# Performance work log

Measured on AMD Instinct MI355X. Metric: run time of the kernel, lower is better.

The kernel has to match this reference:

```python
import jax, jax.numpy as jnp
import numpy as np

B, T, D = 64, 128, 1024
E = 2048      # embedding_dim of state encoder
CD = 256      # VQ code_dim
NC = 1024     # num_codes
BETA = 0.25   # commitment cost


def setup_inputs() -> dict:
    key = jax.random.key(0)
    ks = jax.random.split(key, 5)
    states = jax.random.normal(ks[0], (B, T, D), dtype=jnp.float32)
    next_states = jax.random.normal(ks[1], (B, T, D), dtype=jnp.float32)
    # VarianceScaling(scale=2.0, fan_in) init
    W_s = jax.random.normal(ks[2], (D, E), dtype=jnp.float32) * np.sqrt(2.0 / D)
    b_s = jnp.zeros((E,), dtype=jnp.float32)
    W_p = jax.random.normal(ks[3], (2 * E, CD), dtype=jnp.float32) * np.sqrt(2.0 / (2 * E))
    b_p = jnp.zeros((CD,), dtype=jnp.float32)
    codebook = jax.random.normal(ks[4], (NC, CD), dtype=jnp.float32)
    return {"states": states, "next_states": next_states, "W_s": W_s,
            "b_s": b_s, "W_p": W_p, "b_p": b_p, "codebook": codebook}


def reference(states, next_states, W_s, b_s, W_p, b_p, codebook):
    # dual state encoder (shared weights)
    se = states @ W_s + b_s            # (B,T,E)
    ne = next_states @ W_s + b_s       # (B,T,E)
    policy_input = jax.nn.gelu(jnp.concatenate([se, ne], axis=-1))  # (B,T,2E)
    latent = policy_input @ W_p + b_p  # (B,T,CD)

    # --- VectorQuantizerEMA forward ---
    flat = latent.reshape(-1, CD)      # (N, CD), N = B*T
    # squared euclidean distances to codebook rows
    dists = (jnp.sum(flat * flat, axis=1, keepdims=True)
             - 2.0 * flat @ codebook.T
             + jnp.sum(codebook * codebook, axis=1))  # (N, NC)
    idx = jnp.argmin(dists, axis=1)                    # (N,)
    encodings = jax.nn.one_hot(idx, NC, dtype=latent.dtype)  # (N, NC)
    quantize = codebook[idx].reshape(latent.shape)     # (B,T,CD)

    e_latent_loss = jnp.mean(jnp.square(jax.lax.stop_gradient(quantize) - latent))
    loss = BETA * e_latent_loss
    # straight-through estimator
    quantize_st = latent + jax.lax.stop_gradient(quantize - latent)

    avg_probs = jnp.mean(encodings, axis=0)
    perplexity = jnp.exp(-jnp.sum(avg_probs * jnp.log(avg_probs + 1e-10)))

    encodings = encodings.reshape(B, T, NC)
    encoding_indices = idx.reshape(B, T)
    return quantize_st, loss, perplexity, encodings, encoding_indices
```

## Files before the change

kernel.cpp:

```cpp
#include <hip/hip_runtime.h>

#define NROW  8192
#define D_    1024
#define E_    2048
#define P2E_  4096
#define CD_   256
#define NC_   1024
#define BETA_ 0.25f
#define SPLITK 8

typedef __attribute__((ext_vector_type(8))) short short8;
typedef __attribute__((ext_vector_type(4))) float f32x4;

__device__ __forceinline__ ushort f2bf(float x) {
    union { float f; unsigned u; } v; v.f = x;
    unsigned r = (v.u + 0x7fffu + ((v.u >> 16) & 1u)) >> 16;
    return (ushort)r;
}
__device__ __forceinline__ float bf2f(ushort h) {
    union { unsigned u; float f; } v; v.u = ((unsigned)h) << 16;
    return v.f;
}
__device__ __forceinline__ void split2(float x, ushort& h, ushort& l) {
    h = f2bf(x);
    l = f2bf(x - bf2f(h));
}
__device__ __forceinline__ float gelu_tanh(float x) {
    float x3 = x * x * x;
    return 0.5f * x * (1.0f + tanhf(0.7978845608028654f * (x + 0.044715f * x3)));
}

#define GLD16(gp, lp) __builtin_amdgcn_global_load_lds( \
    (const __attribute__((address_space(1))) void*)(gp), \
    (__attribute__((address_space(3))) void*)(lp), 16, 0, 0)

template<int EPI>
__global__ __launch_bounds__(256)
void gemm_bf16x3(const ushort* __restrict__ Ah, const ushort* __restrict__ Al,
                 const ushort* __restrict__ Bh, const ushort* __restrict__ Bl,
                 int K, int ksteps,
                 const float* __restrict__ bias,
                 float* __restrict__ outF,
                 ushort* __restrict__ oPh, ushort* __restrict__ oPl,
                 const float* __restrict__ cn,
                 float* __restrict__ candv, int* __restrict__ candi)
{
    __shared__ alignas(16) ushort sAh[4096], sAl[4096], sBh[4096], sBl[4096];
    const int t = threadIdx.x;
    const int l = t & 63;
    const int w = t >> 6;
    const int wr = w >> 1, wc = w & 1;

    const int nxy = gridDim.x * gridDim.y;
    const int id  = blockIdx.y * gridDim.x + blockIdx.x;
    const int swz = (id & 7) * (nxy >> 3) + (id >> 3);
    const int bx  = swz % gridDim.x;
    const int by  = swz / gridDim.x;

    const int bm = by * 128;
    const int bn = bx * 128;
    const int kstart = (EPI == 1) ? (int)blockIdx.z * (ksteps * 32) : 0;

    const int srow = t >> 2;
    const int scol = ((t & 3) ^ ((t >> 3) & 3)) * 8;
    const ushort* gAh = Ah + (size_t)(bm + srow) * K + kstart + scol;
    const ushort* gAl = Al + (size_t)(bm + srow) * K + kstart + scol;
    const ushort* gBh = Bh + (size_t)(bn + srow) * K + kstart + scol;
    const ushort* gBl = Bl + (size_t)(bn + srow) * K + kstart + scol;
    const size_t rstep = (size_t)64 * K;
    const int lo0 = t * 8, lo1 = t * 8 + 2048;

    f32x4 acc[4][4];
#pragma unroll
    for (int i = 0; i < 4; i++)
#pragma unroll
        for (int j = 0; j < 4; j++) acc[i][j] = (f32x4)0.0f;

    const int rsw = ((l >> 4) ^ (((l & 15) >> 1) & 3)) * 8;
    const int ar = (wr * 64 + (l & 15)) * 32 + rsw;
    const int br = (wc * 64 + (l & 15)) * 32 + rsw;

#define STAGE8() do { \
        GLD16(gAh, &sAh[lo0]); GLD16(gAh + rstep, &sAh[lo1]); \
        GLD16(gAl, &sAl[lo0]); GLD16(gAl + rstep, &sAl[lo1]); \
        GLD16(gBh, &sBh[lo0]); GLD16(gBh + rstep, &sBh[lo1]); \
        GLD16(gBl, &sBl[lo0]); GLD16(gBl + rstep, &sBl[lo1]); \
    } while (0)

    STAGE8();
    __syncthreads();

    for (int s = 0; s < ksteps; ++s) {
        short8 fah[4], fal[4], fbh[4], fbl[4];
#pragma unroll
        for (int i = 0; i < 4; i++) {
            fah[i] = *(const short8*)&sAh[ar + i * 16 * 32];
            fal[i] = *(const short8*)&sAl[ar + i * 16 * 32];
            fbh[i] = *(const short8*)&sBh[br + i * 16 * 32];
            fbl[i] = *(const short8*)&sBl[br + i * 16 * 32];
        }
        __syncthreads();

        if (s + 1 < ksteps) {
            gAh += 32; gAl += 32; gBh += 32; gBl += 32;
            STAGE8();
        }

        __builtin_amdgcn_s_setprio(1);
#pragma unroll
        for (int i = 0; i < 4; i++)
#pragma unroll
            for (int j = 0; j < 4; j++) {
                acc[i][j] = __builtin_amdgcn_mfma_f32_16x16x32_bf16(fah[i], fbh[j], acc[i][j], 0, 0, 0);
                acc[i][j] = __builtin_amdgcn_mfma_f32_16x16x32_bf16(fah[i], fbl[j], acc[i][j], 0, 0, 0);
                acc[i][j] = __builtin_amdgcn_mfma_f32_16x16x32_bf16(fal[i], fbh[j], acc[i][j], 0, 0, 0);
            }
        __builtin_amdgcn_s_setprio(0);
        __syncthreads();
    }
#undef STAGE8

    if constexpr (EPI == 2) {
        float (*redv)[2] = (float(*)[2])sAh;
        int   (*redi)[2] = (int(*)[2])sAl;
        float cnv[4];
#pragma unroll
        for (int j = 0; j < 4; j++) cnv[j] = cn[bn + wc * 64 + j * 16 + (l & 15)];
#pragma unroll
        for (int i = 0; i < 4; i++) {
            const int grow = bm + wr * 64 + i * 16 + (l >> 4) * 4;
#pragma unroll
            for (int r = 0; r < 4; r++) {
                float bv = INFINITY; int bi = 0;
#pragma unroll
                for (int j = 0; j < 4; j++) {
                    float d = cnv[j] - 2.0f * acc[i][j][r];
                    int c = bn + wc * 64 + j * 16 + (l & 15);
                    if (d < bv) { bv = d; bi = c; }
                }
#pragma unroll
                for (int m = 1; m < 16; m <<= 1) {
                    float ov = __shfl_xor(bv, m, 64);
                    int   oi = __shfl_xor(bi, m, 64);
                    if (ov < bv || (ov == bv && oi < bi)) { bv = ov; bi = oi; }
                }
                int rl = wr * 64 + i * 16 + (l >> 4) * 4 + r;
                if ((l & 15) == 0) { redv[rl][wc] = bv; redi[rl][wc] = bi; }
#pragma unroll
                for (int j = 0; j < 4; j++)
                    outF[(size_t)(grow + r) * NC_ + bn + wc * 64 + j * 16 + (l & 15)] = 0.0f;
            }
        }
        __syncthreads();
        if (t < 128) {
            float v0 = redv[t][0], v1 = redv[t][1];
            int   i0 = redi[t][0], i1 = redi[t][1];
            bool take1 = (v1 < v0) || (v1 == v0 && i1 < i0);
            candv[(size_t)(bm + t) * 8 + bx] = take1 ? v1 : v0;
            candi[(size_t)(bm + t) * 8 + bx] = take1 ? i1 : i0;
        }
        return;
    }

#pragma unroll
    for (int i = 0; i < 4; i++) {
        const int grow = bm + wr * 64 + i * 16 + (l >> 4) * 4;
#pragma unroll
        for (int j = 0; j < 4; j++) {
            const int gcol = bn + wc * 64 + j * 16 + (l & 15);
            f32x4 a = acc[i][j];
            if constexpr (EPI == 0) {
                const float bb = bias[gcol];
#pragma unroll
                for (int r = 0; r < 4; r++) {
                    int m = grow + r;
                    float x = gelu_tanh(a[r] + bb);
                    ushort h, lo; split2(x, h, lo);
                    int pr = (m < NROW) ? m : m - NROW;
                    int pc = ((m < NROW) ? 0 : E_) + gcol;
                    oPh[(size_t)pr * P2E_ + pc] = h;
                    oPl[(size_t)pr * P2E_ + pc] = lo;
                }
            } else if constexpr (EPI == 1) {
                float* o = outF + ((size_t)NROW * blockIdx.z + grow) * CD_ + gcol;
#pragma unroll
                for (int r = 0; r < 4; r++) o[(size_t)r * CD_] = a[r];
            }
        }
    }
}

__global__ void split_k(const float* __restrict__ in, ushort* __restrict__ oh,
                        ushort* __restrict__ ol, int n4)
{
    int i = blockIdx.x * blockDim.x + threadIdx.x;
    int stride = gridDim.x * blockDim.x;
    for (; i < n4; i += stride) {
        float4 v = ((const float4*)in)[i];
        ushort4 h, lo;
        split2(v.x, h.x, lo.x); split2(v.y, h.y, lo.y);
        split2(v.z, h.z, lo.z); split2(v.w, h.w, lo.w);
        ((ushort4*)oh)[i] = h;
        ((ushort4*)ol)[i] = lo;
    }
}

__global__ __launch_bounds__(1024)
void tsplit_k(const float* __restrict__ in, ushort* __restrict__ oh,
              ushort* __restrict__ ol, int R, int C)
{
    __shared__ float tile[32][33];
    int c0 = blockIdx.x * 32, r0 = blockIdx.y * 32;
    int tx = threadIdx.x, ty = threadIdx.y;
    tile[ty][tx] = in[(size_t)(r0 + ty) * C + c0 + tx];
    __syncthreads();
    float x = tile[tx][ty];
    ushort h, lo; split2(x, h, lo);
    size_t o = (size_t)(c0 + ty) * R + r0 + tx;
    oh[o] = h; ol[o] = lo;
}

__global__ __launch_bounds__(256)
void combine_k(const float* __restrict__ part, const float* __restrict__ bias,
               float* __restrict__ latent, ushort* __restrict__ lh,
               ushort* __restrict__ ll)
{
    int row = blockIdx.x, t = threadIdx.x;
    float x = bias[t];
#pragma unroll
    for (int z = 0; z < SPLITK; z++) x += part[((size_t)z * NROW + row) * CD_ + t];
    latent[(size_t)row * CD_ + t] = x;
    ushort h, lo; split2(x, h, lo);
    lh[(size_t)row * CD_ + t] = h;
    ll[(size_t)row * CD_ + t] = lo;
}

__global__ __launch_bounds__(256) void row_norms(const float* __restrict__ X,
                                                 float* __restrict__ out)
{
    __shared__ float s[256];
    int n = blockIdx.x, t = threadIdx.x;
    float v = X[(size_t)n * 256 + t];
    s[t] = v * v;
    __syncthreads();
    for (int st = 128; st > 0; st >>= 1) {
        if (t < st) s[t] += s[t + st];
        __syncthreads();
    }
    if (t == 0) out[n] = s[0];
}

__global__ void zero_hist(int* hist) { hist[threadIdx.x] = 0; }

__global__ __launch_bounds__(256) void vq2_kernel(
    const float* __restrict__ latent, const float* __restrict__ cb,
    const float* __restrict__ candv, const int* __restrict__ candi,
    float* __restrict__ out_enc, float* __restrict__ out_q,
    float* __restrict__ out_idx, int* __restrict__ hist, float* __restrict__ lpart)
{
    __shared__ float sd[256];
    __shared__ int sbc;
    const int n = blockIdx.x, t = threadIdx.x;
    if (t == 0) {
        const float* cv = candv + (size_t)n * 8;
        const int*   ci = candi + (size_t)n * 8;
        float bv = cv[0]; int bi = ci[0];
#pragma unroll
        for (int k = 1; k < 8; k++) {
            float v = cv[k]; int x = ci[k];
            if (v < bv || (v == bv && x < bi)) { bv = v; bi = x; }
        }
        sbc = bi;
    }
    __syncthreads();
    const int bc = sbc;
    if (t == 0) out_enc[(size_t)n * NC_ + bc] = 1.0f;

    float lv = latent[(size_t)n * CD_ + t];
    float q  = cb[(size_t)bc * CD_ + t];
    out_q[(size_t)n * CD_ + t] = lv + (q - lv);
    float diff = q - lv;
    sd[t] = diff * diff;
    __syncthreads();
    for (int st = 128; st > 0; st >>= 1) {
        if (t < st) sd[t] += sd[t + st];
        __syncthreads();
    }
    if (t == 0) {
        lpart[n] = sd[0];
        atomicAdd(&hist[bc], 1);
        out_idx[n] = (float)bc;
    }
}

__global__ __launch_bounds__(1024) void finalize_kernel(
    const float* __restrict__ lpart, const int* __restrict__ hist,
    float* __restrict__ out_loss, float* __restrict__ out_perp)
{
    __shared__ float s[1024];
    int t = threadIdx.x;
    float x = 0.0f;
    for (int i = t; i < NROW; i += 1024) x += lpart[i];
    s[t] = x;
    __syncthreads();
    for (int st = 512; st > 0; st >>= 1) {
        if (t < st) s[t] += s[t + st];
        __syncthreads();
    }
    float total = s[0];
    __syncthreads();
    float p = (float)hist[t] * (1.0f / NROW);
    s[t] = p * logf(p + 1e-10f);
    __syncthreads();
    for (int st = 512; st > 0; st >>= 1) {
        if (t < st) s[t] += s[t + st];
        __syncthreads();
    }
    if (t == 0) {
        *out_loss = BETA_ * (total / (float)((size_t)NROW * CD_));
        *out_perp = expf(-s[0]);
    }
}

extern "C" void kernel_launch(void* const* d_in, const int* in_sizes, int n_in,
                              void* d_out, int out_size, void* d_ws, size_t ws_size,
                              hipStream_t stream)
{
    const float* states      = (const float*)d_in[0];
    const float* next_states = (const float*)d_in[1];
    const float* W_s         = (const float*)d_in[2];
    const float* b_s         = (const float*)d_in[3];
    const float* W_p         = (const float*)d_in[4];
    const float* b_p         = (const float*)d_in[5];
    const float* codebook    = (const float*)d_in[6];

    float* out      = (float*)d_out;
    float* out_q    = out;
    float* out_loss = out + (size_t)NROW * CD_;
    float* out_perp = out_loss + 1;
    float* out_enc  = out_perp + 1;
    float* out_idx  = out_enc + (size_t)NROW * NC_;

    char* ws = (char*)d_ws;
    size_t off = 0;
    auto alloc = [&](size_t bytes) { void* p = ws + off; off += (bytes + 255) & ~255ull; return p; };

    ushort* A1h  = (ushort*)alloc((size_t)2 * NROW * D_ * 2);
    ushort* A1l  = (ushort*)alloc((size_t)2 * NROW * D_ * 2);
    ushort* WsTh = (ushort*)alloc((size_t)E_ * D_ * 2);
    ushort* WsTl = (ushort*)alloc((size_t)E_ * D_ * 2);
    ushort* WpTh = (ushort*)alloc((size_t)CD_ * P2E_ * 2);
    ushort* WpTl = (ushort*)alloc((size_t)CD_ * P2E_ * 2);
    ushort* cbh  = (ushort*)alloc((size_t)NC_ * CD_ * 2);
    ushort* cbl  = (ushort*)alloc((size_t)NC_ * CD_ * 2);
    ushort* Ph   = (ushort*)alloc((size_t)NROW * P2E_ * 2);
    ushort* Pl   = (ushort*)alloc((size_t)NROW * P2E_ * 2);
    ushort* lath = (ushort*)alloc((size_t)NROW * CD_ * 2);
    ushort* latl = (ushort*)alloc((size_t)NROW * CD_ * 2);
    float*  cbn  = (float*)alloc(NC_ * 4);
    int*    hist = (int*)alloc(NC_ * 4);
    float*  lpart= (float*)alloc(NROW * 4);
    float*  candv= (float*)alloc((size_t)NROW * 8 * 4);
    int*    candi= (int*)alloc((size_t)NROW * 8 * 4);
    float* lat_part = (float*)A1h;
    float* latent   = (float*)WsTh;

    {
        int n4 = NROW * D_ / 4;
        split_k<<<2048, 256, 0, stream>>>(states, A1h, A1l, n4);
        split_k<<<2048, 256, 0, stream>>>(next_states, A1h + (size_t)NROW * D_,
                                          A1l + (size_t)NROW * D_, n4);
    }
    tsplit_k<<<dim3(E_ / 32, D_ / 32), dim3(32, 32), 0, stream>>>(W_s, WsTh, WsTl, D_, E_);
    tsplit_k<<<dim3(CD_ / 32, P2E_ / 32), dim3(32, 32), 0, stream>>>(W_p, WpTh, WpTl, P2E_, CD_);
    split_k<<<256, 256, 0, stream>>>(codebook, cbh, cbl, NC_ * CD_ / 4);
    row_norms<<<NC_, 256, 0, stream>>>(codebook, cbn);

    gemm_bf16x3<0><<<dim3(E_ / 128, 2 * NROW / 128), 256, 0, stream>>>(
        A1h, A1l, WsTh, WsTl, D_, D_ / 32, b_s, nullptr, Ph, Pl, nullptr, nullptr, nullptr);

    gemm_bf16x3<1><<<dim3(CD_ / 128, NROW / 128, SPLITK), 256, 0, stream>>>(
        Ph, Pl, WpTh, WpTl, P2E_, P2E_ / 32 / SPLITK, nullptr, lat_part, nullptr, nullptr,
        nullptr, nullptr, nullptr);

    combine_k<<<NROW, 256, 0, stream>>>(lat_part, b_p, latent, lath, latl);

    gemm_bf16x3<2><<<dim3(NC_ / 128, NROW / 128), 256, 0, stream>>>(
        lath, latl, cbh, cbl, CD_, CD_ / 32, nullptr, out_enc, nullptr, nullptr,
        cbn, candv, candi);

    zero_hist<<<1, NC_, 0, stream>>>(hist);
    vq2_kernel<<<NROW, 256, 0, stream>>>(latent, codebook, candv, candi,
                                         out_enc, out_q, out_idx, hist, lpart);
    finalize_kernel<<<1, 1024, 0, stream>>>(lpart, hist, out_loss, out_perp);
}
```

Measured before the change: 359.2 us.

## Widen GEMM tiles to 128x256 with 512 threads and triple-buffered LDS pipeline

Rewrites the split-bf16 GEMM to use 8 waves over a 128x256 output tile and a three-stage LDS ring buffer. Global-to-LDS loads are issued two k-steps ahead and gated with explicit vmcnt waits and raw barriers, replacing the previous single-buffer load/sync pattern. The wider tile also halves the number of argmin candidates per row, so the candidate buffers and the VQ reduction shrink to 4 entries. This is meant to hide memory latency and improve B-tile reuse, at the cost of 144KB of LDS per block and hand-tuned waitcnt values that have to match the number of loads issued.

After: 389.9 us. 1.09x slower.

```diff
diff --git a/kernel.cpp b/kernel.cpp
--- a/kernel.cpp
+++ b/kernel.cpp
@@ -35,21 +35,22 @@
     (__attribute__((address_space(3))) void*)(lp), 16, 0, 0)
 
 template<int EPI>
-__global__ __launch_bounds__(256)
-void gemm_bf16x3(const ushort* __restrict__ Ah, const ushort* __restrict__ Al,
-                 const ushort* __restrict__ Bh, const ushort* __restrict__ Bl,
-                 int K, int ksteps,
-                 const float* __restrict__ bias,
-                 float* __restrict__ outF,
-                 ushort* __restrict__ oPh, ushort* __restrict__ oPl,
-                 const float* __restrict__ cn,
-                 float* __restrict__ candv, int* __restrict__ candi)
-{
-    __shared__ alignas(16) ushort sAh[4096], sAl[4096], sBh[4096], sBl[4096];
+__global__ __launch_bounds__(512, 2)
+void gemm3t(const ushort* __restrict__ Ah, const ushort* __restrict__ Al,
+            const ushort* __restrict__ Bh, const ushort* __restrict__ Bl,
+            int K, int ksteps,
+            const float* __restrict__ bias,
+            float* __restrict__ outF,
+            ushort* __restrict__ oPh, ushort* __restrict__ oPl,
+            const float* __restrict__ cn,
+            float* __restrict__ candv, int* __restrict__ candi)
+{
+    __shared__ alignas(16) ushort lds[3][24576];
     const int t = threadIdx.x;
     const int l = t & 63;
     const int w = t >> 6;
-    const int wr = w >> 1, wc = w & 1;
+    const int wm = w >> 2;
+    const int wn = w & 3;
 
     const int nxy = gridDim.x * gridDim.y;
     const int id  = blockIdx.y * gridDim.x + blockIdx.x;
@@ -58,7 +59,7 @@
     const int by  = swz / gridDim.x;
 
     const int bm = by * 128;
-    const int bn = bx * 128;
+    const int bn = bx * 256;
     const int kstart = (EPI == 1) ? (int)blockIdx.z * (ksteps * 32) : 0;
 
     const int srow = t >> 2;
@@ -67,8 +68,8 @@
     const ushort* gAl = Al + (size_t)(bm + srow) * K + kstart + scol;
     const ushort* gBh = Bh + (size_t)(bn + srow) * K + kstart + scol;
     const ushort* gBl = Bl + (size_t)(bn + srow) * K + kstart + scol;
-    const size_t rstep = (size_t)64 * K;
-    const int lo0 = t * 8, lo1 = t * 8 + 2048;
+    const size_t rstep = (size_t)128 * K;
+    const int d8 = t * 8;
 
     f32x4 acc[4][4];
 #pragma unroll
@@ -76,35 +77,47 @@
 #pragma unroll
         for (int j = 0; j < 4; j++) acc[i][j] = (f32x4)0.0f;
 
-    const int rsw = ((l >> 4) ^ (((l & 15) >> 1) & 3)) * 8;
-    const int ar = (wr * 64 + (l & 15)) * 32 + rsw;
-    const int br = (wc * 64 + (l & 15)) * 32 + rsw;
-
-#define STAGE8() do { \
-        GLD16(gAh, &sAh[lo0]); GLD16(gAh + rstep, &sAh[lo1]); \
-        GLD16(gAl, &sAl[lo0]); GLD16(gAl + rstep, &sAl[lo1]); \
-        GLD16(gBh, &sBh[lo0]); GLD16(gBh + rstep, &sBh[lo1]); \
-        GLD16(gBl, &sBl[lo0]); GLD16(gBl + rstep, &sBl[lo1]); \
+    const int kq = l >> 4, lr = l & 15;
+    const int rsw = (kq ^ ((lr >> 1) & 3)) * 8;
+    int aoff[4], boff[4];
+#pragma unroll
+    for (int i = 0; i < 4; i++) aoff[i] = (wm * 64 + i * 16 + lr) * 32 + rsw;
+#pragma unroll
+    for (int j = 0; j < 4; j++) boff[j] = 8192 + (wn * 64 + j * 16 + lr) * 32 + rsw;
+
+#define STG(b) do { \
+        GLD16(gAh, &lds[b][d8]); \
+        GLD16(gAl, &lds[b][4096 + d8]); \
+        GLD16(gBh, &lds[b][8192 + d8]);  GLD16(gBh + rstep, &lds[b][12288 + d8]); \
+        GLD16(gBl, &lds[b][16384 + d8]); GLD16(gBl + rstep, &lds[b][20480 + d8]); \
+        gAh += 32; gAl += 32; gBh += 32; gBl += 32; \
     } while (0)
 
-    STAGE8();
-    __syncthreads();
-
+    STG(0);
+    STG(1);
     for (int s = 0; s < ksteps; ++s) {
+        const int cb = s % 3;
+        if (s + 2 < ksteps) STG((s + 2) % 3);
+        const int rem = ksteps - 1 - s;
+        if (rem >= 2)      asm volatile("s_waitcnt vmcnt(12)" ::: "memory");
+        else if (rem == 1) asm volatile("s_waitcnt vmcnt(6)"  ::: "memory");
+        else               asm volatile("s_waitcnt vmcnt(0)"  ::: "memory");
+        __builtin_amdgcn_s_barrier();
+        __builtin_amdgcn_sched_barrier(0);
+
         short8 fah[4], fal[4], fbh[4], fbl[4];
 #pragma unroll
         for (int i = 0; i < 4; i++) {
-            fah[i] = *(const short8*)&sAh[ar + i * 16 * 32];
-            fal[i] = *(const short8*)&sAl[ar + i * 16 * 32];
-            fbh[i] = *(const short8*)&sBh[br + i * 16 * 32];
-            fbl[i] = *(const short8*)&sBl[br + i * 16 * 32];
-        }
-        __syncthreads();
-
-        if (s + 1 < ksteps) {
-            gAh += 32; gAl += 32; gBh += 32; gBl += 32;
-            STAGE8();
-        }
+            fah[i] = *(const short8*)&lds[cb][aoff[i]];
+            fal[i] = *(const short8*)&lds[cb][4096 + aoff[i]];
+        }
+#pragma unroll
+        for (int j = 0; j < 4; j++) {
+            fbh[j] = *(const short8*)&lds[cb][boff[j]];
+            fbl[j] = *(const short8*)&lds[cb][8192 + boff[j]];
+        }
+        asm volatile("s_waitcnt lgkmcnt(0)" ::: "memory");
+        __builtin_amdgcn_sched_barrier(0);
 
         __builtin_amdgcn_s_setprio(1);
 #pragma unroll
@@ -116,26 +129,27 @@
                 acc[i][j] = __builtin_amdgcn_mfma_f32_16x16x32_bf16(fal[i], fbh[j], acc[i][j], 0, 0, 0);
             }
         __builtin_amdgcn_s_setprio(0);
-        __syncthreads();
-    }
-#undef STAGE8
+        __builtin_amdgcn_s_barrier();
+        __builtin_amdgcn_sched_barrier(0);
+    }
+#undef STG
 
     if constexpr (EPI == 2) {
-        float (*redv)[2] = (float(*)[2])sAh;
-        int   (*redi)[2] = (int(*)[2])sAl;
+        float (*redv)[4] = (float(*)[4])&lds[0][0];
+        int   (*redi)[4] = (int(*)[4])&lds[0][1024];
         float cnv[4];
 #pragma unroll
-        for (int j = 0; j < 4; j++) cnv[j] = cn[bn + wc * 64 + j * 16 + (l & 15)];
+        for (int j = 0; j < 4; j++) cnv[j] = cn[bn + wn * 64 + j * 16 + lr];
 #pragma unroll
         for (int i = 0; i < 4; i++) {
-            const int grow = bm + wr * 64 + i * 16 + (l >> 4) * 4;
+            const int grow = bm + wm * 64 + i * 16 + kq * 4;
 #pragma unroll
             for (int r = 0; r < 4; r++) {
                 float bv = INFINITY; int bi = 0;
 #pragma unroll
                 for (int j = 0; j < 4; j++) {
                     float d = cnv[j] - 2.0f * acc[i][j][r];
-                    int c = bn + wc * 64 + j * 16 + (l & 15);
+                    int c = bn + wn * 64 + j * 16 + lr;
                     if (d < bv) { bv = d; bi = c; }
                 }
 #pragma unroll
@@ -144,30 +158,33 @@
                     int   oi = __shfl_xor(bi, m, 64);
                     if (ov < bv || (ov == bv && oi < bi)) { bv = ov; bi = oi; }
                 }
-                int rl = wr * 64 + i * 16 + (l >> 4) * 4 + r;
-                if ((l & 15) == 0) { redv[rl][wc] = bv; redi[rl][wc] = bi; }
+                int rl = wm * 64 + i * 16 + kq * 4 + r;
+                if (lr == 0) { redv[rl][wn] = bv; redi[rl][wn] = bi; }
 #pragma unroll
                 for (int j = 0; j < 4; j++)
-                    outF[(size_t)(grow + r) * NC_ + bn + wc * 64 + j * 16 + (l & 15)] = 0.0f;
+                    outF[(size_t)(grow + r) * NC_ + bn + wn * 64 + j * 16 + lr] = 0.0f;
             }
         }
         __syncthreads();
         if (t < 128) {
-            float v0 = redv[t][0], v1 = redv[t][1];
-            int   i0 = redi[t][0], i1 = redi[t][1];
-            bool take1 = (v1 < v0) || (v1 == v0 && i1 < i0);
-            candv[(size_t)(bm + t) * 8 + bx] = take1 ? v1 : v0;
-            candi[(size_t)(bm + t) * 8 + bx] = take1 ? i1 : i0;
+            float bv = redv[t][0]; int bi = redi[t][0];
+#pragma unroll
+            for (int k = 1; k < 4; k++) {
+                float v = redv[t][k]; int x = redi[t][k];
+                if (v < bv || (v == bv && x < bi)) { bv = v; bi = x; }
+            }
+            candv[(size_t)(bm + t) * 4 + bx] = bv;
+            candi[(size_t)(bm + t) * 4 + bx] = bi;
         }
         return;
     }
 
 #pragma unroll
     for (int i = 0; i < 4; i++) {
-        const int grow = bm + wr * 64 + i * 16 + (l >> 4) * 4;
+        const int grow = bm + wm * 64 + i * 16 + kq * 4;
 #pragma unroll
         for (int j = 0; j < 4; j++) {
-            const int gcol = bn + wc * 64 + j * 16 + (l & 15);
+            const int gcol = bn + wn * 64 + j * 16 + lr;
             f32x4 a = acc[i][j];
             if constexpr (EPI == 0) {
                 const float bb = bias[gcol];
@@ -262,11 +279,11 @@
     __shared__ int sbc;
     const int n = blockIdx.x, t = threadIdx.x;
     if (t == 0) {
-        const float* cv = candv + (size_t)n * 8;
-        const int*   ci = candi + (size_t)n * 8;
+        const float* cv = candv + (size_t)n * 4;
+        const int*   ci = candi + (size_t)n * 4;
         float bv = cv[0]; int bi = ci[0];
 #pragma unroll
-        for (int k = 1; k < 8; k++) {
+        for (int k = 1; k < 4; k++) {
             float v = cv[k]; int x = ci[k];
             if (v < bv || (v == bv && x < bi)) { bv = v; bi = x; }
         }
@@ -360,8 +377,8 @@
     float*  cbn  = (float*)alloc(NC_ * 4);
     int*    hist = (int*)alloc(NC_ * 4);
     float*  lpart= (float*)alloc(NROW * 4);
-    float*  candv= (float*)alloc((size_t)NROW * 8 * 4);
-    int*    candi= (int*)alloc((size_t)NROW * 8 * 4);
+    float*  candv= (float*)alloc((size_t)NROW * 4 * 4);
+    int*    candi= (int*)alloc((size_t)NROW * 4 * 4);
     float* lat_part = (float*)A1h;
     float* latent   = (float*)WsTh;
 
@@ -376,16 +393,16 @@
     split_k<<<256, 256, 0, stream>>>(codebook, cbh, cbl, NC_ * CD_ / 4);
     row_norms<<<NC_, 256, 0, stream>>>(codebook, cbn);
 
-    gemm_bf16x3<0><<<dim3(E_ / 128, 2 * NROW / 128), 256, 0, stream>>>(
+    gemm3t<0><<<dim3(E_ / 256, 2 * NROW / 128), 512, 0, stream>>>(
         A1h, A1l, WsTh, WsTl, D_, D_ / 32, b_s, nullptr, Ph, Pl, nullptr, nullptr, nullptr);
 
-    gemm_bf16x3<1><<<dim3(CD_ / 128, NROW / 128, SPLITK), 256, 0, stream>>>(
+    gemm3t<1><<<dim3(1, NROW / 128, SPLITK), 512, 0, stream>>>(
         Ph, Pl, WpTh, WpTl, P2E_, P2E_ / 32 / SPLITK, nullptr, lat_part, nullptr, nullptr,
         nullptr, nullptr, nullptr);
 
     combine_k<<<NROW, 256, 0, stream>>>(lat_part, b_p, latent, lath, latl);
 
-    gemm_bf16x3<2><<<dim3(NC_ / 128, NROW / 128), 256, 0, stream>>>(
+    gemm3t<2><<<dim3(NC_ / 256, NROW / 128), 512, 0, stream>>>(
         lath, latl, cbh, cbl, CD_, CD_ / 32, nullptr, out_enc, nullptr, nullptr,
         cbn, candv, candi);
 
```

## Split GEMM tile across 8 waves with 2x4 wave layout

Applied to the files above, without the earlier changes.

The bf16x3 GEMM kernels now launch 512 threads per 128x128 tile instead of 256. Each wave computes a 64x32 sub-tile instead of 64x64, and each thread stages one 16-byte chunk per operand instead of two. The aim is more waves per CU and fewer accumulator registers per thread, to improve latency hiding. In exchange, each wave re-reads more A fragments from LDS per MFMA, and the argmin reduction in the last GEMM now merges four wave-column partial results.

Result: no change. 361.2 us (+0.6%).

```diff
diff --git a/kernel.cpp b/kernel.cpp
--- a/kernel.cpp
+++ b/kernel.cpp
@@ -35,7 +35,7 @@
     (__attribute__((address_space(3))) void*)(lp), 16, 0, 0)
 
 template<int EPI>
-__global__ __launch_bounds__(256)
+__global__ __launch_bounds__(512, 4)
 void gemm_bf16x3(const ushort* __restrict__ Ah, const ushort* __restrict__ Al,
                  const ushort* __restrict__ Bh, const ushort* __restrict__ Bl,
                  int K, int ksteps,
@@ -49,7 +49,8 @@
     const int t = threadIdx.x;
     const int l = t & 63;
     const int w = t >> 6;
-    const int wr = w >> 1, wc = w & 1;
+    const int wm = w >> 2;
+    const int wn = w & 3;
 
     const int nxy = gridDim.x * gridDim.y;
     const int id  = blockIdx.y * gridDim.x + blockIdx.x;
@@ -67,75 +68,78 @@
     const ushort* gAl = Al + (size_t)(bm + srow) * K + kstart + scol;
     const ushort* gBh = Bh + (size_t)(bn + srow) * K + kstart + scol;
     const ushort* gBl = Bl + (size_t)(bn + srow) * K + kstart + scol;
-    const size_t rstep = (size_t)64 * K;
-    const int lo0 = t * 8, lo1 = t * 8 + 2048;
-
-    f32x4 acc[4][4];
+    const int d8 = t * 8;
+
+    f32x4 acc[4][2];
 #pragma unroll
     for (int i = 0; i < 4; i++)
 #pragma unroll
-        for (int j = 0; j < 4; j++) acc[i][j] = (f32x4)0.0f;
-
-    const int rsw = ((l >> 4) ^ (((l & 15) >> 1) & 3)) * 8;
-    const int ar = (wr * 64 + (l & 15)) * 32 + rsw;
-    const int br = (wc * 64 + (l & 15)) * 32 + rsw;
-
-#define STAGE8() do { \
-        GLD16(gAh, &sAh[lo0]); GLD16(gAh + rstep, &sAh[lo1]); \
-        GLD16(gAl, &sAl[lo0]); GLD16(gAl + rstep, &sAl[lo1]); \
-        GLD16(gBh, &sBh[lo0]); GLD16(gBh + rstep, &sBh[lo1]); \
-        GLD16(gBl, &sBl[lo0]); GLD16(gBl + rstep, &sBl[lo1]); \
+        for (int j = 0; j < 2; j++) acc[i][j] = (f32x4)0.0f;
+
+    const int kq = l >> 4, lr = l & 15;
+    const int rsw = (kq ^ ((lr >> 1) & 3)) * 8;
+    const int abase = (wm * 64 + lr) * 32 + rsw;
+    const int bbase = (wn * 32 + lr) * 32 + rsw;
+
+#define STAGE4() do { \
+        GLD16(gAh, &sAh[d8]); GLD16(gAl, &sAl[d8]); \
+        GLD16(gBh, &sBh[d8]); GLD16(gBl, &sBl[d8]); \
     } while (0)
 
-    STAGE8();
+    STAGE4();
     __syncthreads();
 
     for (int s = 0; s < ksteps; ++s) {
-        short8 fah[4], fal[4], fbh[4], fbl[4];
+        short8 fbh[2], fbl[2];
+#pragma unroll
+        for (int j = 0; j < 2; j++) {
+            fbh[j] = *(const short8*)&sBh[bbase + j * 16 * 32];
+            fbl[j] = *(const short8*)&sBl[bbase + j * 16 * 32];
+        }
+        short8 fah[4], fal[4];
 #pragma unroll
         for (int i = 0; i < 4; i++) {
-            fah[i] = *(const short8*)&sAh[ar + i * 16 * 32];
-            fal[i] = *(const short8*)&sAl[ar + i * 16 * 32];
-            fbh[i] = *(const short8*)&sBh[br + i * 16 * 32];
-            fbl[i] = *(const short8*)&sBl[br + i * 16 * 32];
+            fah[i] = *(const short8*)&sAh[abase + i * 16 * 32];
+            fal[i] = *(const short8*)&sAl[abase + i * 16 * 32];
         }
         __syncthreads();
 
         if (s + 1 < ksteps) {
             gAh += 32; gAl += 32; gBh += 32; gBl += 32;
-            STAGE8();
+            STAGE4();
         }
 
         __builtin_amdgcn_s_setprio(1);
 #pragma unroll
-        for (int i = 0; i < 4; i++)
-#pragma unroll
-            for (int j = 0; j < 4; j++) {
+        for (int i = 0; i < 4; i++) {
+#pragma unroll
+            for (int j = 0; j < 2; j++) {
                 acc[i][j] = __builtin_amdgcn_mfma_f32_16x16x32_bf16(fah[i], fbh[j], acc[i][j], 0, 0, 0);
                 acc[i][j] = __builtin_amdgcn_mfma_f32_16x16x32_bf16(fah[i], fbl[j], acc[i][j], 0, 0, 0);
                 acc[i][j] = __builtin_amdgcn_mfma_f32_16x16x32_bf16(fal[i], fbh[j], acc[i][j], 0, 0, 0);
             }
+        }
         __builtin_amdgcn_s_setprio(0);
         __syncthreads();
     }
-#undef STAGE8
+#undef STAGE4
 
     if constexpr (EPI == 2) {
-        float (*redv)[2] = (float(*)[2])sAh;
-        int   (*redi)[2] = (int(*)[2])sAl;
-        float cnv[4];
-#pragma unroll
-        for (int j = 0; j < 4; j++) cnv[j] = cn[bn + wc * 64 + j * 16 + (l & 15)];
+        float (*redv)[4] = (float(*)[4])sAh;
+        int   (*redi)[4] = (int(*)[4])sAl;
+        float cnv[2];
+#pragma unroll
+        for (int j = 0; j < 2; j++) cnv[j] = cn[bn + wn * 32 + j * 16 + lr];
 #pragma unroll
         for (int i = 0; i < 4; i++) {
-            const int grow = bm + wr * 64 + i * 16 + (l >> 4) * 4;
+            const int grow = bm + wm * 64 + i * 16 + kq * 4;
 #pragma unroll
             for (int r = 0; r < 4; r++) {
                 float bv = INFINITY; int bi = 0;
 #pragma unroll
-                for (int j = 0; j < 4; j++) {
+                for (int j = 0; j < 2; j++) {
                     float d = cnv[j] - 2.0f * acc[i][j][r];
-                    int c = bn + wc * 64 + j * 16 + (l & 15);
+                    int c = bn + wn * 32 + j * 16 + lr;
                     if (d < bv) { bv = d; bi = c; }
                 }
 #pragma unroll
@@ -144,30 +148,33 @@
                     int   oi = __shfl_xor(bi, m, 64);
                     if (ov < bv || (ov == bv && oi < bi)) { bv = ov; bi = oi; }
                 }
-                int rl = wr * 64 + i * 16 + (l >> 4) * 4 + r;
-                if ((l & 15) == 0) { redv[rl][wc] = bv; redi[rl][wc] = bi; }
-#pragma unroll
-                for (int j = 0; j < 4; j++)
-                    outF[(size_t)(grow + r) * NC_ + bn + wc * 64 + j * 16 + (l & 15)] = 0.0f;
+                int rl = wm * 64 + i * 16 + kq * 4 + r;
+                if (lr == 0) { redv[rl][wn] = bv; redi[rl][wn] = bi; }
+#pragma unroll
+                for (int j = 0; j < 2; j++)
+                    outF[(size_t)(grow + r) * NC_ + bn + wn * 32 + j * 16 + lr] = 0.0f;
             }
         }
         __syncthreads();
         if (t < 128) {
-            float v0 = redv[t][0], v1 = redv[t][1];
-            int   i0 = redi[t][0], i1 = redi[t][1];
-            bool take1 = (v1 < v0) || (v1 == v0 && i1 < i0);
-            candv[(size_t)(bm + t) * 8 + bx] = take1 ? v1 : v0;
-            candi[(size_t)(bm + t) * 8 + bx] = take1 ? i1 : i0;
+            float bv = redv[t][0]; int bi = redi[t][0];
+#pragma unroll
+            for (int k = 1; k < 4; k++) {
+                float v = redv[t][k]; int x = redi[t][k];
+                if (v < bv || (v == bv && x < bi)) { bv = v; bi = x; }
+            }
+            candv[(size_t)(bm + t) * 8 + bx] = bv;
+            candi[(size_t)(bm + t) * 8 + bx] = bi;
         }
         return;
     }
 
 #pragma unroll
     for (int i = 0; i < 4; i++) {
-        const int grow = bm + wr * 64 + i * 16 + (l >> 4) * 4;
-#pragma unroll
-        for (int j = 0; j < 4; j++) {
-            const int gcol = bn + wc * 64 + j * 16 + (l & 15);
+        const int grow = bm + wm * 64 + i * 16 + kq * 4;
+#pragma unroll
+        for (int j = 0; j < 2; j++) {
+            const int gcol = bn + wn * 32 + j * 16 + lr;
             f32x4 a = acc[i][j];
             if constexpr (EPI == 0) {
                 const float bb = bias[gcol];
@@ -376,16 +383,16 @@
     split_k<<<256, 256, 0, stream>>>(codebook, cbh, cbl, NC_ * CD_ / 4);
     row_norms<<<NC_, 256, 0, stream>>>(codebook, cbn);
 
-    gemm_bf16x3<0><<<dim3(E_ / 128, 2 * NROW / 128), 256, 0, stream>>>(
+    gemm_bf16x3<0><<<dim3(E_ / 128, 2 * NROW / 128), 512, 0, stream>>>(
         A1h, A1l, WsTh, WsTl, D_, D_ / 32, b_s, nullptr, Ph, Pl, nullptr, nullptr, nullptr);
 
-    gemm_bf16x3<1><<<dim3(CD_ / 128, NROW / 128, SPLITK), 256, 0, stream>>>(
+    gemm_bf16x3<1><<<dim3(CD_ / 128, NROW / 128, SPLITK), 512, 0, stream>>>(
         Ph, Pl, WpTh, WpTl, P2E_, P2E_ / 32 / SPLITK, nullptr, lat_part, nullptr, nullptr,
         nullptr, nullptr, nullptr);
 
     combine_k<<<NROW, 256, 0, stream>>>(lat_part, b_p, latent, lath, latl);
 
-    gemm_bf16x3<2><<<dim3(NC_ / 128, NROW / 128), 256, 0, stream>>>(
+    gemm_bf16x3<2><<<dim3(NC_ / 128, NROW / 128), 512, 0, stream>>>(
         lath, latl, cbh, cbl, CD_, CD_ / 32, nullptr, out_enc, nullptr, nullptr,
         cbn, candv, candi);
 
```

## Load B operand fragments directly from global into registers, double-buffered

Applied to the files above, without the earlier changes.

The B tile (hi and lo bf16 parts) is no longer staged through LDS. Each wave reads its B MFMA fragments straight from global memory into registers, using two register buffers that alternate across k-steps, while A still goes through LDS. This halves shared memory use and adds a launch-bounds occupancy hint so three blocks can fit per CU. The cost is that B rows shared by the waves in a block are fetched redundantly from global/L2, register pressure rises, and the loop now assumes an even number of k-steps.

Measured after the change: 548.6 us. +52.7%, slower.

```diff
diff --git a/kernel.cpp b/kernel.cpp
--- a/kernel.cpp
+++ b/kernel.cpp
@@ -35,7 +35,7 @@
     (__attribute__((address_space(3))) void*)(lp), 16, 0, 0)
 
 template<int EPI>
-__global__ __launch_bounds__(256)
+__global__ __launch_bounds__(256, 3)
 void gemm_bf16x3(const ushort* __restrict__ Ah, const ushort* __restrict__ Al,
                  const ushort* __restrict__ Bh, const ushort* __restrict__ Bl,
                  int K, int ksteps,
@@ -45,7 +45,7 @@
                  const float* __restrict__ cn,
                  float* __restrict__ candv, int* __restrict__ candi)
 {
-    __shared__ alignas(16) ushort sAh[4096], sAl[4096], sBh[4096], sBl[4096];
+    __shared__ alignas(16) ushort sAh[4096], sAl[4096];
     const int t = threadIdx.x;
     const int l = t & 63;
     const int w = t >> 6;
@@ -65,77 +65,100 @@
     const int scol = ((t & 3) ^ ((t >> 3) & 3)) * 8;
     const ushort* gAh = Ah + (size_t)(bm + srow) * K + kstart + scol;
     const ushort* gAl = Al + (size_t)(bm + srow) * K + kstart + scol;
-    const ushort* gBh = Bh + (size_t)(bn + srow) * K + kstart + scol;
-    const ushort* gBl = Bl + (size_t)(bn + srow) * K + kstart + scol;
     const size_t rstep = (size_t)64 * K;
     const int lo0 = t * 8, lo1 = t * 8 + 2048;
 
+    const int kq = l >> 4, lr = l & 15;
+    const ushort* pBh = Bh + (size_t)(bn + wc * 64 + lr) * K + kstart + kq * 8;
+    const ushort* pBl = Bl + (size_t)(bn + wc * 64 + lr) * K + kstart + kq * 8;
+
     f32x4 acc[4][4];
 #pragma unroll
     for (int i = 0; i < 4; i++)
 #pragma unroll
         for (int j = 0; j < 4; j++) acc[i][j] = (f32x4)0.0f;
 
-    const int rsw = ((l >> 4) ^ (((l & 15) >> 1) & 3)) * 8;
-    const int ar = (wr * 64 + (l & 15)) * 32 + rsw;
-    const int br = (wc * 64 + (l & 15)) * 32 + rsw;
-
-#define STAGE8() do { \
-        GLD16(gAh, &sAh[lo0]); GLD16(gAh + rstep, &sAh[lo1]); \
-        GLD16(gAl, &sAl[lo0]); GLD16(gAl + rstep, &sAl[lo1]); \
-        GLD16(gBh, &sBh[lo0]); GLD16(gBh + rstep, &sBh[lo1]); \
-        GLD16(gBl, &sBl[lo0]); GLD16(gBl + rstep, &sBl[lo1]); \
+    const int rsw = (kq ^ ((lr >> 1) & 3)) * 8;
+    const int ar = (wr * 64 + lr) * 32 + rsw;
+
+    short8 b0h[4], b0l[4], b1h[4], b1l[4];
+
+#define STAGEA(koff) do { \
+        GLD16(gAh + (koff), &sAh[lo0]); GLD16(gAh + (koff) + rstep, &sAh[lo1]); \
+        GLD16(gAl + (koff), &sAl[lo0]); GLD16(gAl + (koff) + rstep, &sAl[lo1]); \
     } while (0)
-
-    STAGE8();
-    __syncthreads();
-
-    for (int s = 0; s < ksteps; ++s) {
-        short8 fah[4], fal[4], fbh[4], fbl[4];
-#pragma unroll
-        for (int i = 0; i < 4; i++) {
-            fah[i] = *(const short8*)&sAh[ar + i * 16 * 32];
-            fal[i] = *(const short8*)&sAl[ar + i * 16 * 32];
-            fbh[i] = *(const short8*)&sBh[br + i * 16 * 32];
-            fbl[i] = *(const short8*)&sBl[br + i * 16 * 32];
-        }
-        __syncthreads();
-
-        if (s + 1 < ksteps) {
-            gAh += 32; gAl += 32; gBh += 32; gBl += 32;
-            STAGE8();
-        }
-
-        __builtin_amdgcn_s_setprio(1);
-#pragma unroll
-        for (int i = 0; i < 4; i++)
-#pragma unroll
-            for (int j = 0; j < 4; j++) {
-                acc[i][j] = __builtin_amdgcn_mfma_f32_16x16x32_bf16(fah[i], fbh[j], acc[i][j], 0, 0, 0);
-                acc[i][j] = __builtin_amdgcn_mfma_f32_16x16x32_bf16(fah[i], fbl[j], acc[i][j], 0, 0, 0);
-                acc[i][j] = __builtin_amdgcn_mfma_f32_16x16x32_bf16(fal[i], fbh[j], acc[i][j], 0, 0, 0);
+#define LOADB(bh, bl, koff) do { \
+        _Pragma("unroll") \
+        for (int j = 0; j < 4; j++) { \
+            bh[j] = *(const short8*)(pBh + (size_t)j * 16 * K + (koff)); \
+            bl[j] = *(const short8*)(pBl + (size_t)j * 16 * K + (koff)); \
+        } } while (0)
+#define LDA() do { \
+        _Pragma("unroll") \
+        for (int i = 0; i < 4; i++) { \
+            fah[i] = *(const short8*)&sAh[ar + i * 16 * 32]; \
+            fal[i] = *(const short8*)&sAl[ar + i * 16 * 32]; \
+        } } while (0)
+#define MFMA3(bh, bl) do { \
+        __builtin_amdgcn_s_setprio(1); \
+        _Pragma("unroll") \
+        for (int i = 0; i < 4; i++) \
+            _Pragma("unroll") \
+            for (int j = 0; j < 4; j++) { \
+                acc[i][j] = __builtin_amdgcn_mfma_f32_16x16x32_bf16(fah[i], bh[j], acc[i][j], 0, 0, 0); \
+                acc[i][j] = __builtin_amdgcn_mfma_f32_16x16x32_bf16(fah[i], bl[j], acc[i][j], 0, 0, 0); \
+                acc[i][j] = __builtin_amdgcn_mfma_f32_16x16x32_bf16(fal[i], bh[j], acc[i][j], 0, 0, 0); \
+            } \
+        __builtin_amdgcn_s_setprio(0); \
+    } while (0)
+
+    LOADB(b0h, b0l, 0);
+    STAGEA(0);
+    __syncthreads();
+
+    for (int s = 0; s < ksteps; s += 2) {
+        {
+            short8 fah[4], fal[4];
+            LDA();
+            __syncthreads();
+            STAGEA((s + 1) * 32);
+            LOADB(b1h, b1l, (s + 1) * 32);
+            MFMA3(b0h, b0l);
+            __syncthreads();
+        }
+        {
+            short8 fah[4], fal[4];
+            LDA();
+            __syncthreads();
+            if (s + 2 < ksteps) {
+                STAGEA((s + 2) * 32);
+                LOADB(b0h, b0l, (s + 2) * 32);
             }
-        __builtin_amdgcn_s_setprio(0);
-        __syncthreads();
-    }
-#undef STAGE8
+            MFMA3(b1h, b1l);
+            __syncthreads();
+        }
+    }
+#undef STAGEA
+#undef LOADB
+#undef LDA
+#undef MFMA3
 
     if constexpr (EPI == 2) {
         float (*redv)[2] = (float(*)[2])sAh;
         int   (*redi)[2] = (int(*)[2])sAl;
         float cnv[4];
 #pragma unroll
-        for (int j = 0; j < 4; j++) cnv[j] = cn[bn + wc * 64 + j * 16 + (l & 15)];
+        for (int j = 0; j < 4; j++) cnv[j] = cn[bn + wc * 64 + j * 16 + lr];
 #pragma unroll
         for (int i = 0; i < 4; i++) {
-            const int grow = bm + wr * 64 + i * 16 + (l >> 4) * 4;
+            const int grow = bm + wr * 64 + i * 16 + kq * 4;
 #pragma unroll
             for (int r = 0; r < 4; r++) {
                 float bv = INFINITY; int bi = 0;
 #pragma unroll
                 for (int j = 0; j < 4; j++) {
                     float d = cnv[j] - 2.0f * acc[i][j][r];
-                    int c = bn + wc * 64 + j * 16 + (l & 15);
+                    int c = bn + wc * 64 + j * 16 + lr;
                     if (d < bv) { bv = d; bi = c; }
                 }
 #pragma unroll
@@ -144,11 +167,11 @@
                     int   oi = __shfl_xor(bi, m, 64);
                     if (ov < bv || (ov == bv && oi < bi)) { bv = ov; bi = oi; }
                 }
-                int rl = wr * 64 + i * 16 + (l >> 4) * 4 + r;
-                if ((l & 15) == 0) { redv[rl][wc] = bv; redi[rl][wc] = bi; }
+                int rl = wr * 64 + i * 16 + kq * 4 + r;
+                if (lr == 0) { redv[rl][wc] = bv; redi[rl][wc] = bi; }
 #pragma unroll
                 for (int j = 0; j < 4; j++)
-                    outF[(size_t)(grow + r) * NC_ + bn + wc * 64 + j * 16 + (l & 15)] = 0.0f;
+                    outF[(size_t)(grow + r) * NC_ + bn + wc * 64 + j * 16 + lr] = 0.0f;
             }
         }
         __syncthreads();
@@ -164,10 +187,10 @@
 
 #pragma unroll
     for (int i = 0; i < 4; i++) {
-        const int grow = bm + wr * 64 + i * 16 + (l >> 4) * 4;
+        const int grow = bm + wr * 64 + i * 16 + kq * 4;
 #pragma unroll
         for (int j = 0; j < 4; j++) {
-            const int gcol = bn + wc * 64 + j * 16 + (l & 15);
+            const int gcol = bn + wc * 64 + j * 16 + lr;
             f32x4 a = acc[i][j];
             if constexpr (EPI == 0) {
                 const float bb = bias[gcol];
```
